# Kernel tuning notes

Measured on AMD Instinct MI355X. Metric: run time of the kernel, lower is better.

## Reference

```python
import jax, jax.numpy as jnp
import numpy as np

D = 1024
H = 16
DH = D // H  # 64


def setup_inputs() -> dict:
    key = jax.random.key(0)
    ks = jax.random.split(key, 7)
    B, S = 2, 2048
    X = jax.random.normal(ks[0], (B, S, D), dtype=jnp.float32)
    s = 1.0 / np.sqrt(D)
    # per-head projection weights stacked over heads: [H, D, DH]
    Wq = jax.random.normal(ks[1], (H, D, DH), dtype=jnp.float32) * s
    Wk = jax.random.normal(ks[2], (H, D, DH), dtype=jnp.float32) * s
    Wv = jax.random.normal(ks[3], (H, D, DH), dtype=jnp.float32) * s
    bq = jax.random.normal(ks[4], (H, DH), dtype=jnp.float32) * s
    bk = jax.random.normal(ks[5], (H, DH), dtype=jnp.float32) * s
    bv = jax.random.normal(ks[6], (H, DH), dtype=jnp.float32) * s
    return {"X": X, "Wq": Wq, "Wk": Wk, "Wv": Wv, "bq": bq, "bk": bk, "bv": bv}


def reference(X, Wq, Wk, Wv, bq, bk, bv):
    B, S, _ = X.shape
    scale = jnp.sqrt(jnp.float32(DH))
    # per-head QKV projections, vectorized over heads: [B, H, S, DH]
    Q = jnp.einsum('bsd,hde->bhse', X, Wq) + bq[None, :, None, :]
    K = jnp.einsum('bsd,hde->bhse', X, Wk) + bk[None, :, None, :]
    V = jnp.einsum('bsd,hde->bhse', X, Wv) + bv[None, :, None, :]
    # full dense scores (the original materializes them): [B, H, S, S]
    QK = jnp.einsum('bhqe,bhke->bhqk', Q, K) / scale
    # NOTE: faithful to source — softmax over full row FIRST, then tril mask
    # applied AFTER softmax (rows are NOT renormalized).
    sQK = jax.nn.softmax(QK, axis=-1) * jnp.tril(jnp.ones((S, S), dtype=QK.dtype))
    Z = jnp.einsum('bhqk,bhke->bhqe', sQK, V)  # [B, H, S, DH]
    # concat heads along feature dim in head order
    return Z.transpose(0, 2, 1, 3).reshape(B, S, H * DH)
```

## Files before the change

### kernel.cpp

```cpp
#include <hip/hip_runtime.h>
#include <hip/hip_bf16.h>
#include <hip/hip_fp16.h>

#define DD   1024
#define HH   16
#define DHH  64
#define SS   2048
#define BB   2

using f32x4 = __attribute__((ext_vector_type(4))) float;
using s16x8 = __attribute__((ext_vector_type(8))) short;
using s16x4 = __attribute__((ext_vector_type(4))) short;
using f16x8 = __attribute__((ext_vector_type(8))) _Float16;
using u32x4 = __attribute__((ext_vector_type(4))) unsigned;

#if __has_builtin(__builtin_amdgcn_exp2f)
#define EXP2(x) __builtin_amdgcn_exp2f(x)
#else
#define EXP2(x) exp2f(x)
#endif

static __device__ __forceinline__ short f2h(float x) {
    _Float16 h = (_Float16)x;
    return __builtin_bit_cast(short, h);
}
static __device__ __forceinline__ unsigned pk2(float a, float b) {
    auto h = __builtin_amdgcn_cvt_pkrtz(a, b);
    return __builtin_bit_cast(unsigned, h);
}

static __device__ __forceinline__ void glds16(const void* g, void* l) {
    __builtin_amdgcn_global_load_lds(
        (const __attribute__((address_space(1))) unsigned int*)g,
        (__attribute__((address_space(3))) unsigned int*)l, 16, 0, 0);
}

static __device__ __forceinline__ int swz(int row, int blk) {
    return row * 128 + (((blk) ^ (row & 7)) << 4);
}

static __device__ __forceinline__ f32x4 MFMA16(s16x8 a, s16x8 b, f32x4 c) {
    return __builtin_amdgcn_mfma_f32_16x16x32_f16(
        __builtin_bit_cast(f16x8, a), __builtin_bit_cast(f16x8, b), c, 0, 0, 0);
}

#define QSCALE 0.18033688011112042f

#define WT_OFF 0u
#define VT_OFF 6291456u
#define QH_OFF 14680064u
#define KH_OFF 23068672u
#define XH_OFF 31457280u

__global__ __launch_bounds__(256) void prep_kernel(
    const float* __restrict__ X,
    const float* __restrict__ Wq, const float* __restrict__ Wk, const float* __restrict__ Wv,
    short* __restrict__ XhG, short* __restrict__ WtG)
{
    __shared__ float Ws[64][65];
    const int t = threadIdx.x;

    if (blockIdx.x < 2048) {
        size_t base = ((size_t)blockIdx.x * 256 + t) * 8;
        float4 a = *(const float4*)(X + base);
        float4 b = *(const float4*)(X + base + 4);
        s16x8 hv;
        hv[0] = f2h(a.x); hv[1] = f2h(a.y); hv[2] = f2h(a.z); hv[3] = f2h(a.w);
        hv[4] = f2h(b.x); hv[5] = f2h(b.y); hv[6] = f2h(b.z); hv[7] = f2h(b.w);
        *(s16x8*)(XhG + base) = hv;
        return;
    }

    const int bid = blockIdx.x - 2048;
    const int dt = bid & 15;
    const int mh = bid >> 4;
    const int mat = mh >> 4, h = mh & 15;
    const int d0 = dt * 64;
    const float* Wm = (mat == 0 ? Wq : (mat == 1 ? Wk : Wv)) + (size_t)h * DD * DHH;

#pragma unroll
    for (int i = 0; i < 4; i++) {
        int f = t + 256 * i;
        int row = f >> 4;
        int c4  = f & 15;
        float4 v = *(const float4*)(Wm + (size_t)(d0 + row) * DHH + c4 * 4);
        Ws[row][c4 * 4 + 0] = v.x;
        Ws[row][c4 * 4 + 1] = v.y;
        Ws[row][c4 * 4 + 2] = v.z;
        Ws[row][c4 * 4 + 3] = v.w;
    }
    __syncthreads();

    const int e = t >> 2, dq = t & 3;
    s16x8 h0, h1;
#pragma unroll
    for (int i = 0; i < 8; i++) h0[i] = f2h(Ws[dq * 16 + i][e]);
#pragma unroll
    for (int i = 0; i < 8; i++) h1[i] = f2h(Ws[dq * 16 + 8 + i][e]);
    size_t off = ((size_t)(mh * 64 + e)) * DD + d0 + dq * 16;
    *(s16x8*)(WtG + off)     = h0;
    *(s16x8*)(WtG + off + 8) = h1;
}

__global__ __launch_bounds__(256, 2) void proj_kernel(
    const short* __restrict__ XhG,
    const short* __restrict__ WtG,
    const float* __restrict__ bq, const float* __restrict__ bk,
    const float* __restrict__ bv,
    short* __restrict__ QhG, short* __restrict__ KhG, short* __restrict__ VtG)
{
    const int s0 = blockIdx.x * 128;
    const int y  = blockIdx.y;
    const bool isV = (y >= 16);
    const int n0 = isV ? (y - 16) * 128 : y * 128;
    const size_t wrow0 = (size_t)(isV ? 2048 + n0 : n0);

    __shared__ __align__(16) char smem[32768];
    const int WT = 0, XT = 16384;

    const int t = threadIdx.x;
    const int w = t >> 6, lane = t & 63, g = lane >> 4, ln = lane & 15;
    const int wm = w >> 1, wn = w & 1;

    const char* Abase = smem + (isV ? XT : WT);
    const char* Bbase = smem + (isV ? WT : XT);

    f32x4 acc[4][4];
#pragma unroll
    for (int i = 0; i < 4; i++)
#pragma unroll
        for (int j = 0; j < 4; j++) acc[i][j] = (f32x4){0.f, 0.f, 0.f, 0.f};

    for (int d0 = 0; d0 < DD; d0 += 64) {
        if (d0) __syncthreads();
#pragma unroll
        for (int p = 0; p < 4; p++) {
            int idx = p * 256 + t;
            int row = idx >> 3, blk = idx & 7;
            int soff = (blk ^ (row & 7)) * 8;
            glds16(WtG + (wrow0 + row) * DD + d0 + soff, smem + WT + idx * 16);
            glds16(XhG + (size_t)(s0 + row) * DD + d0 + soff, smem + XT + idx * 16);
        }
        __syncthreads();

        s16x8 bfr[4][2];
#pragma unroll
        for (int nf = 0; nf < 4; nf++)
#pragma unroll
            for (int kst = 0; kst < 2; kst++)
                bfr[nf][kst] = *(const s16x8*)(Bbase + swz(64 * wn + nf * 16 + ln, kst * 4 + g));
#pragma unroll
        for (int mf = 0; mf < 4; mf++) {
            s16x8 afr[2];
#pragma unroll
            for (int kst = 0; kst < 2; kst++)
                afr[kst] = *(const s16x8*)(Abase + swz(64 * wm + mf * 16 + ln, kst * 4 + g));
#pragma unroll
            for (int kst = 0; kst < 2; kst++)
#pragma unroll
                for (int nf = 0; nf < 4; nf++)
                    acc[mf][nf] = MFMA16(afr[kst], bfr[nf][kst], acc[mf][nf]);
        }
    }

    if (!isV) {
        const int mat = n0 >> 10;
        const int h = ((n0 + 64 * wm) >> 6) & 15;
        const float* bptr = (mat ? bk : bq) + h * 64;
        short* OutP = mat ? KhG : QhG;
        const float scale = mat ? 1.0f : QSCALE;
#pragma unroll
        for (int nf = 0; nf < 4; nf++) {
            int sg = s0 + 64 * wn + nf * 16 + ln;
            int bidx = sg >> 11, sr = sg & (SS - 1);
            size_t rowbase = ((size_t)((bidx * HH + h) * SS + sr)) * DHH;
#pragma unroll
            for (int mf = 0; mf < 4; mf++) {
                float4 bias = *(const float4*)(bptr + mf * 16 + g * 4);
                float bb[4] = {bias.x, bias.y, bias.z, bias.w};
                s16x4 h4;
#pragma unroll
                for (int r = 0; r < 4; r++) h4[r] = f2h((acc[mf][nf][r] + bb[r]) * scale);
                *(s16x4*)(OutP + rowbase + mf * 16 + g * 4) = h4;
            }
        }
    } else {
        const int h = ((n0 + 64 * wn) >> 6) & 15;
#pragma unroll
        for (int nf = 0; nf < 4; nf++) {
            int e = nf * 16 + ln;
            float bvv = bv[h * 64 + e];
#pragma unroll
            for (int mf = 0; mf < 4; mf++) {
                int sgb = s0 + 64 * wm + mf * 16 + g * 4;
                int bidx = sgb >> 11, sr = sgb & (SS - 1);
                s16x4 v4;
#pragma unroll
                for (int r = 0; r < 4; r++) v4[r] = f2h(acc[mf][nf][r] + bvv);
                size_t base = ((size_t)(bidx * HH + h)) * (SS * DHH);
                int idx = ((((((sr >> 6) * 2 + ((sr >> 5) & 1)) * 4 + nf) * 4
                            + ((sr >> 3) & 3)) * 16 + ln) << 3) + (sr & 7);
                *(s16x4*)(VtG + base + idx) = v4;
            }
        }
    }
}

__global__ __launch_bounds__(256, 4) void attn_kernel(
    const short* __restrict__ QhG, const short* __restrict__ KhG,
    const short* __restrict__ VtG,
    float* __restrict__ out)
{
    const int wid = (blockIdx.x & 7) * 128 + (blockIdx.x >> 3);
    const int qraw = wid & 31, h = (wid >> 5) & 15, b = wid >> 9;
    const int qt = ((wid >> 5) & 1) ? (31 - qraw) : qraw;
    const int q0 = qt * 64;
    const size_t ho = (size_t)(b * HH + h) * SS * DHH;

    __shared__ __align__(16) char smem[32768];

    const int t = threadIdx.x;
    const int w = t >> 6, lane = t & 63, g = lane >> 4, ln = lane & 15;
    const int qrow = 16 * w + ln;
    const int qg = q0 + qrow;

    s16x8 qh[2];
#pragma unroll
    for (int kst = 0; kst < 2; kst++)
        qh[kst] = *(const s16x8*)(QhG + ho + (size_t)qg * DHH + kst * 32 + g * 8);

    int soffA[4], krowA[4];
#pragma unroll
    for (int p = 0; p < 4; p++) {
        int idx = p * 256 + t;
        int row = idx >> 3, blk = idx & 7;
        int lrow = row & 63, sub = row >> 6;
        soffA[p] = (blk ^ (lrow & 7)) * 8;
        krowA[p] = sub * 64
                 + ((lrow >> 5) & 1) * 32 + ((lrow >> 2) & 3) * 8
                 + ((lrow >> 4) & 1) * 4 + (lrow & 3);
    }

    auto stageK = [&](int buf, int it) {
        const int k0s = it * 128;
#pragma unroll
        for (int p = 0; p < 4; p++) {
            int idx = p * 256 + t;
            glds16(KhG + ho + (size_t)(k0s + krowA[p]) * DHH + soffA[p],
                   smem + buf * 16384 + idx * 16);
        }
    };

    stageK(0, 0);

    f32x4 o[4];
#pragma unroll
    for (int i = 0; i < 4; i++) o[i] = (f32x4){0.f, 0.f, 0.f, 0.f};
    float lpart = 0.f;

    int cur = 0;
    for (int it = 0; it < SS / 128; it++) {
        __syncthreads();
        if (it < SS / 128 - 1) stageK(cur ^ 1, it + 1);
        const char* Kbase = smem + cur * 16384;

#pragma unroll 1
        for (int ss = 0; ss < 2; ss++) {
            const int kt2 = it * 2 + ss;
            const int k0 = kt2 * 64;
            const bool do_pv = (kt2 <= qt);

            s16x8 av[4][2];
            if (do_pv) {
#pragma unroll
                for (int mf = 0; mf < 4; mf++)
#pragma unroll
                    for (int kst = 0; kst < 2; kst++)
                        av[mf][kst] = *(const s16x8*)(VtG + ho +
                            ((((((size_t)kt2 * 2 + kst) * 4 + mf) * 4 + g) * 16 + ln) << 3));
            }

            f32x4 s[4];
#pragma unroll
            for (int i = 0; i < 4; i++) s[i] = (f32x4){0.f, 0.f, 0.f, 0.f};

            const char* Kb = Kbase + ss * 8192;
#pragma unroll
            for (int kst = 0; kst < 2; kst++) {
                s16x8 ak[4];
#pragma unroll
                for (int mf = 0; mf < 4; mf++)
                    ak[mf] = *(const s16x8*)(Kb + swz(mf * 16 + ln, kst * 4 + g));
#pragma unroll
                for (int mf = 0; mf < 4; mf++)
                    s[mf] = MFMA16(ak[mf], qh[kst], s[mf]);
            }

#pragma unroll
            for (int mf = 0; mf < 4; mf++)
#pragma unroll
                for (int r = 0; r < 4; r++)
                    s[mf][r] = EXP2(s[mf][r]);
            {
                float p0 = (s[0][0] + s[0][1]) + (s[0][2] + s[0][3]);
                float p1 = (s[1][0] + s[1][1]) + (s[1][2] + s[1][3]);
                float p2 = (s[2][0] + s[2][1]) + (s[2][2] + s[2][3]);
                float p3 = (s[3][0] + s[3][1]) + (s[3][2] + s[3][3]);
                lpart += (p0 + p1) + (p2 + p3);
            }

            if (do_pv) {
                const bool diag = (kt2 == qt);
#pragma unroll
                for (int kst = 0; kst < 2; kst++) {
                    u32x4 u;
                    if (diag) {
                        int kb = k0 + kst * 32 + g * 8;
                        float pa[4], pb[4];
#pragma unroll
                        for (int r = 0; r < 4; r++) {
                            pa[r] = (kb + r     > qg) ? 0.f : s[2 * kst][r];
                            pb[r] = (kb + 4 + r > qg) ? 0.f : s[2 * kst + 1][r];
                        }
                        u.x = pk2(pa[0], pa[1]); u.y = pk2(pa[2], pa[3]);
                        u.z = pk2(pb[0], pb[1]); u.w = pk2(pb[2], pb[3]);
                    } else {
                        u.x = pk2(s[2 * kst][0], s[2 * kst][1]);
                        u.y = pk2(s[2 * kst][2], s[2 * kst][3]);
                        u.z = pk2(s[2 * kst + 1][0], s[2 * kst + 1][1]);
                        u.w = pk2(s[2 * kst + 1][2], s[2 * kst + 1][3]);
                    }
                    s16x8 bp = __builtin_bit_cast(s16x8, u);
#pragma unroll
                    for (int mf = 0; mf < 4; mf++)
                        o[mf] = MFMA16(av[mf][kst], bp, o[mf]);
                }
            }
        }
        cur ^= 1;
    }

    {
        float l = lpart;
        l += __shfl_xor(l, 16);
        l += __shfl_xor(l, 32);
        float inv = 1.0f / l;
        float* op = out + ((size_t)(b * SS + qg)) * (HH * DHH) + h * DHH;
#pragma unroll
        for (int mf = 0; mf < 4; mf++) {
            float4 vv = {o[mf][0] * inv, o[mf][1] * inv,
                         o[mf][2] * inv, o[mf][3] * inv};
            *(float4*)(op + mf * 16 + g * 4) = vv;
        }
    }
}

extern "C" void kernel_launch(void* const* d_in, const int* in_sizes, int n_in,
                              void* d_out, int out_size, void* d_ws, size_t ws_size,
                              hipStream_t stream) {
    const float* X  = (const float*)d_in[0];
    const float* Wq = (const float*)d_in[1];
    const float* Wk = (const float*)d_in[2];
    const float* Wv = (const float*)d_in[3];
    const float* bq = (const float*)d_in[4];
    const float* bk = (const float*)d_in[5];
    const float* bv = (const float*)d_in[6];
    float* out = (float*)d_out;

    char* wsb = (char*)d_ws;
    short* Wt = (short*)(wsb + WT_OFF);
    short* Vt = (short*)(wsb + VT_OFF);
    short* Qh = (short*)(wsb + QH_OFF);
    short* Kh = (short*)(wsb + KH_OFF);
    short* Xh = (short*)(wsb + XH_OFF);

    prep_kernel<<<2816, 256, 0, stream>>>(X, Wq, Wk, Wv, Xh, Wt);
    proj_kernel<<<dim3(32, 24), 256, 0, stream>>>(Xh, Wt, bq, bk, bv, Qh, Kh, Vt);
    attn_kernel<<<1024, 256, 0, stream>>>(Qh, Kh, Vt, out);
}
```

Before: 85.98 us.

## Store K in MFMA fragment order and load directly from global, dropping LDS staging

The projection kernel now writes K in a pre-swizzled fragment layout matching the MFMA operand order, like V already was. The attention kernel then reads K fragments straight from global memory with coalesced 16-byte loads, removing the LDS double buffer, the glds staging and the per-iteration __syncthreads. This drops shared memory use, which may raise occupancy, and removes barrier stalls. In exchange each of the four waves reloads the same K tile from global/L2 instead of sharing it through LDS, which raises cache traffic and exposes load latency without explicit prefetch.

Result: slower. 101.2 us (+17.7%).

```diff
diff --git a/kernel.cpp b/kernel.cpp
--- a/kernel.cpp
+++ b/kernel.cpp
@@ -49,7 +49,7 @@
 #define WT_OFF 0u
 #define VT_OFF 6291456u
 #define QH_OFF 14680064u
-#define KH_OFF 23068672u
+#define KT_OFF 23068672u
 #define XH_OFF 31457280u
 
 __global__ __launch_bounds__(256) void prep_kernel(
@@ -107,7 +107,7 @@
     const short* __restrict__ WtG,
     const float* __restrict__ bq, const float* __restrict__ bk,
     const float* __restrict__ bv,
-    short* __restrict__ QhG, short* __restrict__ KhG, short* __restrict__ VtG)
+    short* __restrict__ QhG, short* __restrict__ KtG, short* __restrict__ VtG)
 {
     const int s0 = blockIdx.x * 128;
     const int y  = blockIdx.y;
@@ -167,21 +167,38 @@
         const int mat = n0 >> 10;
         const int h = ((n0 + 64 * wm) >> 6) & 15;
         const float* bptr = (mat ? bk : bq) + h * 64;
-        short* OutP = mat ? KhG : QhG;
-        const float scale = mat ? 1.0f : QSCALE;
 #pragma unroll
         for (int nf = 0; nf < 4; nf++) {
             int sg = s0 + 64 * wn + nf * 16 + ln;
             int bidx = sg >> 11, sr = sg & (SS - 1);
-            size_t rowbase = ((size_t)((bidx * HH + h) * SS + sr)) * DHH;
-#pragma unroll
-            for (int mf = 0; mf < 4; mf++) {
-                float4 bias = *(const float4*)(bptr + mf * 16 + g * 4);
-                float bb[4] = {bias.x, bias.y, bias.z, bias.w};
-                s16x4 h4;
-#pragma unroll
-                for (int r = 0; r < 4; r++) h4[r] = f2h((acc[mf][nf][r] + bb[r]) * scale);
-                *(s16x4*)(OutP + rowbase + mf * 16 + g * 4) = h4;
+            if (mat == 0) {
+                size_t rowbase = ((size_t)((bidx * HH + h) * SS + sr)) * DHH;
+#pragma unroll
+                for (int mf = 0; mf < 4; mf++) {
+                    float4 bias = *(const float4*)(bptr + mf * 16 + g * 4);
+                    float bb[4] = {bias.x, bias.y, bias.z, bias.w};
+                    s16x4 h4;
+#pragma unroll
+                    for (int r = 0; r < 4; r++) h4[r] = f2h((acc[mf][nf][r] + bb[r]) * QSCALE);
+                    *(s16x4*)(QhG + rowbase + mf * 16 + g * 4) = h4;
+                }
+            } else {
+                size_t base = ((size_t)(bidx * HH + h)) * (SS * DHH);
+                int kt2  = sr >> 6;
+                int sr63 = sr & 63;
+                int mfa = ((sr63 >> 5) & 1) * 2 + ((sr63 >> 2) & 1);
+                int lna = ((sr63 >> 3) & 3) * 4 + (sr63 & 3);
+#pragma unroll
+                for (int mf = 0; mf < 4; mf++) {
+                    float4 bias = *(const float4*)(bptr + mf * 16 + g * 4);
+                    float bb[4] = {bias.x, bias.y, bias.z, bias.w};
+                    s16x4 h4;
+#pragma unroll
+                    for (int r = 0; r < 4; r++) h4[r] = f2h(acc[mf][nf][r] + bb[r]);
+                    int idx = (((((kt2 * 2 + (mf >> 1)) * 4 + mfa) * 4
+                               + ((mf & 1) * 2 + (g >> 1))) * 16 + lna) << 3) + (g & 1) * 4;
+                    *(s16x4*)(KtG + base + idx) = h4;
+                }
             }
         }
     } else {
@@ -207,7 +224,7 @@
 }
 
 __global__ __launch_bounds__(256, 4) void attn_kernel(
-    const short* __restrict__ QhG, const short* __restrict__ KhG,
+    const short* __restrict__ QhG, const short* __restrict__ KtG,
     const short* __restrict__ VtG,
     float* __restrict__ out)
 {
@@ -217,8 +234,6 @@
     const int q0 = qt * 64;
     const size_t ho = (size_t)(b * HH + h) * SS * DHH;
 
-    __shared__ __align__(16) char smem[32768];
-
     const int t = threadIdx.x;
     const int w = t >> 6, lane = t & 63, g = lane >> 4, ln = lane & 15;
     const int qrow = 16 * w + ln;
@@ -229,115 +244,84 @@
     for (int kst = 0; kst < 2; kst++)
         qh[kst] = *(const s16x8*)(QhG + ho + (size_t)qg * DHH + kst * 32 + g * 8);
 
-    int soffA[4], krowA[4];
-#pragma unroll
-    for (int p = 0; p < 4; p++) {
-        int idx = p * 256 + t;
-        int row = idx >> 3, blk = idx & 7;
-        int lrow = row & 63, sub = row >> 6;
-        soffA[p] = (blk ^ (lrow & 7)) * 8;
-        krowA[p] = sub * 64
-                 + ((lrow >> 5) & 1) * 32 + ((lrow >> 2) & 3) * 8
-                 + ((lrow >> 4) & 1) * 4 + (lrow & 3);
-    }
-
-    auto stageK = [&](int buf, int it) {
-        const int k0s = it * 128;
-#pragma unroll
-        for (int p = 0; p < 4; p++) {
-            int idx = p * 256 + t;
-            glds16(KhG + ho + (size_t)(k0s + krowA[p]) * DHH + soffA[p],
-                   smem + buf * 16384 + idx * 16);
-        }
-    };
-
-    stageK(0, 0);
-
     f32x4 o[4];
 #pragma unroll
     for (int i = 0; i < 4; i++) o[i] = (f32x4){0.f, 0.f, 0.f, 0.f};
     float lpart = 0.f;
 
-    int cur = 0;
-    for (int it = 0; it < SS / 128; it++) {
-        __syncthreads();
-        if (it < SS / 128 - 1) stageK(cur ^ 1, it + 1);
-        const char* Kbase = smem + cur * 16384;
-
-#pragma unroll 1
-        for (int ss = 0; ss < 2; ss++) {
-            const int kt2 = it * 2 + ss;
-            const int k0 = kt2 * 64;
-            const bool do_pv = (kt2 <= qt);
-
-            s16x8 av[4][2];
-            if (do_pv) {
+    const int laneoff = (g * 16 + ln) * 8;
+
+    for (int kt = 0; kt < SS / 64; kt++) {
+        const int k0 = kt * 64;
+        const bool do_pv = (kt <= qt);
+
+        s16x8 ak[4][2];
+#pragma unroll
+        for (int mf = 0; mf < 4; mf++)
+#pragma unroll
+            for (int kst = 0; kst < 2; kst++)
+                ak[mf][kst] = *(const s16x8*)(KtG + ho +
+                    ((size_t)((kt * 2 + kst) * 4 + mf) << 9) + laneoff);
+
+        s16x8 av[4][2];
+        if (do_pv) {
+#pragma unroll
+            for (int mf = 0; mf < 4; mf++)
+#pragma unroll
+                for (int kst = 0; kst < 2; kst++)
+                    av[mf][kst] = *(const s16x8*)(VtG + ho +
+                        ((size_t)((kt * 2 + kst) * 4 + mf) << 9) + laneoff);
+        }
+
+        f32x4 s[4];
+#pragma unroll
+        for (int i = 0; i < 4; i++) s[i] = (f32x4){0.f, 0.f, 0.f, 0.f};
+#pragma unroll
+        for (int kst = 0; kst < 2; kst++)
+#pragma unroll
+            for (int mf = 0; mf < 4; mf++)
+                s[mf] = MFMA16(ak[mf][kst], qh[kst], s[mf]);
+
+#pragma unroll
+        for (int mf = 0; mf < 4; mf++)
+#pragma unroll
+            for (int r = 0; r < 4; r++)
+                s[mf][r] = EXP2(s[mf][r]);
+        {
+            float p0 = (s[0][0] + s[0][1]) + (s[0][2] + s[0][3]);
+            float p1 = (s[1][0] + s[1][1]) + (s[1][2] + s[1][3]);
+            float p2 = (s[2][0] + s[2][1]) + (s[2][2] + s[2][3]);
+            float p3 = (s[3][0] + s[3][1]) + (s[3][2] + s[3][3]);
+            lpart += (p0 + p1) + (p2 + p3);
+        }
+
+        if (do_pv) {
+            const bool diag = (kt == qt);
+#pragma unroll
+            for (int kst = 0; kst < 2; kst++) {
+                u32x4 u;
+                if (diag) {
+                    int kb = k0 + kst * 32 + g * 8;
+                    float pa[4], pb[4];
+#pragma unroll
+                    for (int r = 0; r < 4; r++) {
+                        pa[r] = (kb + r     > qg) ? 0.f : s[2 * kst][r];
+                        pb[r] = (kb + 4 + r > qg) ? 0.f : s[2 * kst + 1][r];
+                    }
+                    u.x = pk2(pa[0], pa[1]); u.y = pk2(pa[2], pa[3]);
+                    u.z = pk2(pb[0], pb[1]); u.w = pk2(pb[2], pb[3]);
+                } else {
+                    u.x = pk2(s[2 * kst][0], s[2 * kst][1]);
+                    u.y = pk2(s[2 * kst][2], s[2 * kst][3]);
+                    u.z = pk2(s[2 * kst + 1][0], s[2 * kst + 1][1]);
+                    u.w = pk2(s[2 * kst + 1][2], s[2 * kst + 1][3]);
+                }
+                s16x8 bp = __builtin_bit_cast(s16x8, u);
 #pragma unroll
                 for (int mf = 0; mf < 4; mf++)
-#pragma unroll
-                    for (int kst = 0; kst < 2; kst++)
-                        av[mf][kst] = *(const s16x8*)(VtG + ho +
-                            ((((((size_t)kt2 * 2 + kst) * 4 + mf) * 4 + g) * 16 + ln) << 3));
+                    o[mf] = MFMA16(av[mf][kst], bp, o[mf]);
             }
-
-            f32x4 s[4];
-#pragma unroll
-            for (int i = 0; i < 4; i++) s[i] = (f32x4){0.f, 0.f, 0.f, 0.f};
-
-            const char* Kb = Kbase + ss * 8192;
-#pragma unroll
-            for (int kst = 0; kst < 2; kst++) {
-                s16x8 ak[4];
-#pragma unroll
-                for (int mf = 0; mf < 4; mf++)
-                    ak[mf] = *(const s16x8*)(Kb + swz(mf * 16 + ln, kst * 4 + g));
-#pragma unroll
-                for (int mf = 0; mf < 4; mf++)
-                    s[mf] = MFMA16(ak[mf], qh[kst], s[mf]);
-            }
-
-#pragma unroll
-            for (int mf = 0; mf < 4; mf++)
-#pragma unroll
-                for (int r = 0; r < 4; r++)
-                    s[mf][r] = EXP2(s[mf][r]);
-            {
-                float p0 = (s[0][0] + s[0][1]) + (s[0][2] + s[0][3]);
-                float p1 = (s[1][0] + s[1][1]) + (s[1][2] + s[1][3]);
-                float p2 = (s[2][0] + s[2][1]) + (s[2][2] + s[2][3]);
-                float p3 = (s[3][0] + s[3][1]) + (s[3][2] + s[3][3]);
-                lpart += (p0 + p1) + (p2 + p3);
-            }
-
-            if (do_pv) {
-                const bool diag = (kt2 == qt);
-#pragma unroll
-                for (int kst = 0; kst < 2; kst++) {
-                    u32x4 u;
-                    if (diag) {
-                        int kb = k0 + kst * 32 + g * 8;
-                        float pa[4], pb[4];
-#pragma unroll
-                        for (int r = 0; r < 4; r++) {
-                            pa[r] = (kb + r     > qg) ? 0.f : s[2 * kst][r];
-                            pb[r] = (kb + 4 + r > qg) ? 0.f : s[2 * kst + 1][r];
-                        }
-                        u.x = pk2(pa[0], pa[1]); u.y = pk2(pa[2], pa[3]);
-                        u.z = pk2(pb[0], pb[1]); u.w = pk2(pb[2], pb[3]);
-                    } else {
-                        u.x = pk2(s[2 * kst][0], s[2 * kst][1]);
-                        u.y = pk2(s[2 * kst][2], s[2 * kst][3]);
-                        u.z = pk2(s[2 * kst + 1][0], s[2 * kst + 1][1]);
-                        u.w = pk2(s[2 * kst + 1][2], s[2 * kst + 1][3]);
-                    }
-                    s16x8 bp = __builtin_bit_cast(s16x8, u);
-#pragma unroll
-                    for (int mf = 0; mf < 4; mf++)
-                        o[mf] = MFMA16(av[mf][kst], bp, o[mf]);
-                }
-            }
-        }
-        cur ^= 1;
+        }
     }
 
     {
@@ -371,10 +355,10 @@
     short* Wt = (short*)(wsb + WT_OFF);
     short* Vt = (short*)(wsb + VT_OFF);
     short* Qh = (short*)(wsb + QH_OFF);
-    short* Kh = (short*)(wsb + KH_OFF);
+    short* Kt = (short*)(wsb + KT_OFF);
     short* Xh = (short*)(wsb + XH_OFF);
 
     prep_kernel<<<2816, 256, 0, stream>>>(X, Wq, Wk, Wv, Xh, Wt);
-    proj_kernel<<<dim3(32, 24), 256, 0, stream>>>(Xh, Wt, bq, bk, bv, Qh, Kh, Vt);
-    attn_kernel<<<1024, 256, 0, stream>>>(Qh, Kh, Vt, out);
-}
+    proj_kernel<<<dim3(32, 24), 256, 0, stream>>>(Xh, Wt, bq, bk, bv, Qh, Kt, Vt);
+    attn_kernel<<<1024, 256, 0, stream>>>(Qh, Kt, Vt, out);
+}
```
